# Optimization experiments

Measured on AMD Instinct MI355X. Metric: run time of the kernel, lower is better.

Reference implementation:

```python
import jax, jax.numpy as jnp
import numpy as np

N, E = 50000, 800000          # nodes, edges
DIN, HEAD, HD = 128, 4, 16    # input dim, heads, per-head dim
DOUT = HEAD * HD              # 64 = head*hd
NEG_SLOPE = 0.01              # torch LeakyReLU default


def _lin(key, fan_in, fan_out):
    # torch nn.Linear default init: U(-1/sqrt(fan_in), 1/sqrt(fan_in))
    kw, kb = jax.random.split(key)
    s = 1.0 / np.sqrt(fan_in)
    W = jax.random.uniform(kw, (fan_in, fan_out), jnp.float32, -s, s)
    b = jax.random.uniform(kb, (fan_out,), jnp.float32, -s, s)
    return W, b


def setup_inputs() -> dict:
    key = jax.random.key(0)
    ks = jax.random.split(key, 8)
    x = jax.random.normal(ks[0], (N, DIN), jnp.float32)
    src = jax.random.randint(ks[1], (E,), 0, N, jnp.int32)
    dst = jax.random.randint(ks[2], (E,), 0, N, jnp.int32)
    Ws, bs = _lin(ks[3], DIN, DOUT)   # relation_aware src linear
    Wd, bd = _lin(ks[4], DIN, DOUT)   # relation_aware dst linear
    Wl, bl = _lin(ks[5], DIN, DOUT)   # w_liner
    Wa, ba = _lin(ks[6], 3 * HD, 1)   # atten
    return dict(x=x, src=src, dst=dst, Ws=Ws, bs=bs, Wd=Wd, bd=bd,
                Wl=Wl, bl=bl, Wa=Wa, ba=ba)


def reference(x, src, dst, Ws, bs, Wd, bd, Wl, bl, Wa, ba):
    # sign_edges: relation-aware per-edge feature edge_sum  [E, DOUT]
    er = jnp.tanh(x[src] @ Ws + bs + (x[dst] @ Wd + bd))

    # w_liner on node features  [N, DOUT]
    h = x @ Wl + bl

    # message: per-edge, per-head concat + linear + leakyrelu score
    sf = h[src].reshape(E, HEAD, HD)
    df = h[dst].reshape(E, HEAD, HD)
    ef = er.reshape(E, HEAD, HD)
    z = jnp.concatenate([sf, df, ef], axis=-1)        # [E, HEAD, 3*HD]
    a = z @ Wa + ba                                    # [E, HEAD, 1]
    a = jnp.where(a >= 0, a, NEG_SLOPE * a)            # leaky relu

    # reduce: mailbox softmax over incoming edges of each dst node
    m = jax.ops.segment_max(a, dst, num_segments=N)    # [N, HEAD, 1]
    m = jnp.where(jnp.isfinite(m), m, 0.0)             # empty mailboxes -> 0
    e = jnp.exp(a - m[dst])
    s = jax.ops.segment_sum(e, dst, num_segments=N)    # [N, HEAD, 1]
    attn = e / jnp.maximum(s[dst], 1e-38)

    out = jax.ops.segment_sum(attn * sf, dst, num_segments=N)
    out = out.reshape(N, DOUT)                         # [N, head*hd]

    # edge_s: mean of edge_sum over incoming edges per node
    deg = jax.ops.segment_sum(jnp.ones((E, 1), x.dtype), dst, num_segments=N)
    edge_s = jax.ops.segment_sum(er, dst, num_segments=N) / jnp.maximum(deg, 1.0)

    return (edge_s, out, h)  # if_sum=False branch: h already [N, head*hd]
```

## Files before the change

### kernel.cpp

```cpp
#include <hip/hip_runtime.h>
#include <math.h>

#define DIN   128
#define DOUT  64
#define NHEAD 4
#define HD    16

typedef __attribute__((ext_vector_type(8))) short bf16x8;
typedef __attribute__((ext_vector_type(8))) unsigned short u16x8;
typedef __attribute__((ext_vector_type(4))) float f32x4;

__device__ __forceinline__ unsigned short f2bf(float f) {
    union { float f; unsigned u; } v; v.f = f;
    unsigned r = v.u + 0x7FFF + ((v.u >> 16) & 1);
    return (unsigned short)(r >> 16);
}
__device__ __forceinline__ float bf2f(unsigned short s) {
    union { unsigned u; float f; } v; v.u = ((unsigned)s) << 16; return v.f;
}

__global__ __launch_bounds__(256)
void k_prep(const float* __restrict__ Ws, const float* __restrict__ Wd,
            const float* __restrict__ Wl, short* __restrict__ wT,
            int* __restrict__ degi, int N) {
    const int idx = blockIdx.x * 256 + threadIdx.x;
    if (idx < 192 * 128) {
        const int n = idx >> 7, k = idx & 127;
        float v;
        if (n < 64)       v = Ws[k * DOUT + n];
        else if (n < 128) v = Wd[k * DOUT + (n - 64)];
        else              v = Wl[k * DOUT + (n - 128)];
        wT[idx] = (short)f2bf(v);
    }
    if (idx < N) degi[idx] = 0;
}

__global__ __launch_bounds__(64)
void k_node_proj(const float* __restrict__ x, const short* __restrict__ wT,
                 const float* __restrict__ bs, const float* __restrict__ bd,
                 const float* __restrict__ bl, const float* __restrict__ Wa,
                 unsigned short* __restrict__ packed_bf,
                 float* __restrict__ xd,
                 float* __restrict__ alpha_s, float* __restrict__ alpha_d,
                 float* __restrict__ h_out, int N) {
    __shared__ short xs[16 * 136];
    const int lane = threadIdx.x;
    const int lam = lane & 15, g = lane >> 4;
    const int n0 = blockIdx.x * 16;

    {
        const int r = lane >> 2, c0 = (lane & 3) * 32;
        const int nn = n0 + r;
#pragma unroll
        for (int j = 0; j < 8; ++j) {
            float4 v = make_float4(0.f, 0.f, 0.f, 0.f);
            if (nn < N) v = ((const float4*)x)[(size_t)nn * 32 + (c0 >> 2) + j];
            short4 h4;
            h4.x = (short)f2bf(v.x); h4.y = (short)f2bf(v.y);
            h4.z = (short)f2bf(v.z); h4.w = (short)f2bf(v.w);
            *(short4*)&xs[r * 136 + c0 + j * 4] = h4;
        }
    }
    __syncthreads();

    bf16x8 afr[4];
#pragma unroll
    for (int ks = 0; ks < 4; ++ks)
        afr[ks] = *(const bf16x8*)&xs[lam * 136 + ks * 32 + g * 8];

    f32x4 acc[12];
#pragma unroll
    for (int c = 0; c < 12; ++c) acc[c] = (f32x4){0.f, 0.f, 0.f, 0.f};

#pragma unroll
    for (int c = 0; c < 12; ++c) {
#pragma unroll
        for (int ks = 0; ks < 4; ++ks) {
            const bf16x8 b = *(const bf16x8*)&wT[(c * 16 + lam) * 128 + ks * 32 + g * 8];
            acc[c] = __builtin_amdgcn_mfma_f32_16x16x32_bf16(afr[ks], b, acc[c], 0, 0, 0);
        }
    }

    float bsv[4], bdv[4], blv[4];
#pragma unroll
    for (int c = 0; c < 4; ++c) {
        bsv[c] = bs[c * 16 + lam];
        bdv[c] = bd[c * 16 + lam];
        blv[c] = bl[c * 16 + lam];
    }
    const float waS = Wa[lam], waD = Wa[16 + lam];
    const int cc_base = (lam >> 2), t_sl = lam & 3;

#pragma unroll
    for (int i = 0; i < 4; ++i) {
        const int node = n0 + g * 4 + i;
        float xsv[4], xdv[4], hv[4];
#pragma unroll
        for (int c = 0; c < 4; ++c) {
            xsv[c] = acc[c][i]     + bsv[c];
            xdv[c] = acc[4 + c][i] + bdv[c];
            hv[c]  = acc[8 + c][i] + blv[c];
        }
        float p0 = hv[0] * waS, p1 = hv[1] * waS, p2 = hv[2] * waS, p3 = hv[3] * waS;
        float q0 = hv[0] * waD, q1 = hv[1] * waD, q2 = hv[2] * waD, q3 = hv[3] * waD;
#pragma unroll
        for (int off = 1; off < 16; off <<= 1) {
            p0 += __shfl_xor(p0, off); p1 += __shfl_xor(p1, off);
            p2 += __shfl_xor(p2, off); p3 += __shfl_xor(p3, off);
            q0 += __shfl_xor(q0, off); q1 += __shfl_xor(q1, off);
            q2 += __shfl_xor(q2, off); q3 += __shfl_xor(q3, off);
        }
        if (node < N) {
            const size_t rowb = (size_t)node * 128;
#pragma unroll
            for (int c = 0; c < 4; ++c) {
                const int cc = c * 4 + cc_base;
                packed_bf[rowb + cc * 8 + t_sl]     = f2bf(xsv[c]);
                packed_bf[rowb + cc * 8 + 4 + t_sl] = f2bf(hv[c]);
                xd   [(size_t)node * DOUT + c * 16 + lam] = xdv[c];
                h_out[(size_t)node * DOUT + c * 16 + lam] = hv[c];
            }
            if (lam == 0) {
                *(f32x4*)&alpha_s[(size_t)node * NHEAD] = (f32x4){p0, p1, p2, p3};
                *(f32x4*)&alpha_d[(size_t)node * NHEAD] = (f32x4){q0, q1, q2, q3};
            }
        }
    }
}

__global__ __launch_bounds__(256)
void k_hist(const int* __restrict__ dst, int* __restrict__ degi,
            int* __restrict__ rank, int E) {
    const int e0 = (blockIdx.x * 256 + threadIdx.x) * 4;
    if (e0 + 3 < E) {
        const int4 d = *(const int4*)&dst[e0];
        int4 r;
        r.x = atomicAdd(&degi[d.x], 1);
        r.y = atomicAdd(&degi[d.y], 1);
        r.z = atomicAdd(&degi[d.z], 1);
        r.w = atomicAdd(&degi[d.w], 1);
        *(int4*)&rank[e0] = r;
    } else {
        for (int e = e0; e < E; ++e) rank[e] = atomicAdd(&degi[dst[e]], 1);
    }
}

__global__ __launch_bounds__(1024)
void k_scan_block(const int* __restrict__ degi, int* __restrict__ excl,
                  int* __restrict__ bsum, int N) {
    __shared__ int wsum[16];
    const int tid = threadIdx.x, lane = tid & 63, wid = tid >> 6;
    const int i = blockIdx.x * 1024 + tid;
    int v = (i < N) ? degi[i] : 0;
    int incl = v;
#pragma unroll
    for (int off = 1; off < 64; off <<= 1) {
        int t = __shfl_up(incl, off);
        if (lane >= off) incl += t;
    }
    if (lane == 63) wsum[wid] = incl;
    __syncthreads();
    if (tid < 16) {
        int t = wsum[tid];
#pragma unroll
        for (int off = 1; off < 16; off <<= 1) {
            int u = __shfl_up(t, off);
            if (tid >= off) t += u;
        }
        wsum[tid] = t;
    }
    __syncthreads();
    const int base = (wid > 0) ? wsum[wid - 1] : 0;
    if (i < N) excl[i] = incl - v + base;
    if (tid == 1023) bsum[blockIdx.x] = wsum[15];
}

__global__ __launch_bounds__(1024)
void k_scan_bsum(const int* __restrict__ bsum, int* __restrict__ boff,
                 int* __restrict__ total, int nb) {
    __shared__ int wsum[16];
    const int tid = threadIdx.x, lane = tid & 63, wid = tid >> 6;
    int v = (tid < nb) ? bsum[tid] : 0;
    int incl = v;
#pragma unroll
    for (int off = 1; off < 64; off <<= 1) {
        int t = __shfl_up(incl, off);
        if (lane >= off) incl += t;
    }
    if (lane == 63) wsum[wid] = incl;
    __syncthreads();
    if (tid < 16) {
        int t = wsum[tid];
#pragma unroll
        for (int off = 1; off < 16; off <<= 1) {
            int u = __shfl_up(t, off);
            if (tid >= off) t += u;
        }
        wsum[tid] = t;
    }
    __syncthreads();
    const int base = (wid > 0) ? wsum[wid - 1] : 0;
    if (tid < nb) boff[tid] = incl - v + base;
    if (tid == 1023) *total = wsum[15];
}

__global__ __launch_bounds__(256)
void k_scatter(const int* __restrict__ src, const int* __restrict__ dst,
               const int* __restrict__ rp_raw, const int* __restrict__ boff,
               const int* __restrict__ rank, int* __restrict__ srcs_sorted, int E) {
    const int e0 = (blockIdx.x * 256 + threadIdx.x) * 4;
    if (e0 + 3 < E) {
        const int4 s = *(const int4*)&src[e0];
        const int4 d = *(const int4*)&dst[e0];
        const int4 r = *(const int4*)&rank[e0];
        srcs_sorted[rp_raw[d.x] + boff[d.x >> 10] + r.x] = s.x;
        srcs_sorted[rp_raw[d.y] + boff[d.y >> 10] + r.y] = s.y;
        srcs_sorted[rp_raw[d.z] + boff[d.z >> 10] + r.z] = s.z;
        srcs_sorted[rp_raw[d.w] + boff[d.w >> 10] + r.w] = s.w;
    } else {
        for (int e = e0; e < E; ++e) {
            const int d = dst[e];
            srcs_sorted[rp_raw[d] + boff[d >> 10] + rank[e]] = src[e];
        }
    }
}

__global__ __launch_bounds__(256, 8)
void k_aggregate(const int* __restrict__ rp_raw, const int* __restrict__ boff,
                 const int* __restrict__ total, const int* __restrict__ srcs,
                 const unsigned short* __restrict__ packed_bf,
                 const float* __restrict__ xd,
                 const float* __restrict__ alpha_s, const float* __restrict__ alpha_d,
                 const float* __restrict__ Wa, const float* __restrict__ ba,
                 float* __restrict__ edge_s, float* __restrict__ out, int N) {
    const int lane = threadIdx.x & 63;
    const int n = blockIdx.x * 4 + (threadIdx.x >> 6);
    if (n >= N) return;
    const int g = lane >> 4, lam = lane & 15;
    const int hd = lam >> 2, q = lam & 3;

    const int start = rp_raw[n] + boff[n >> 10];
    const int end = (n + 1 < N) ? (rp_raw[n + 1] + boff[(n + 1) >> 10]) : *total;
    const int deg = end - start;
    const int last = end - 1;

    const float4 xd4 = *(const float4*)&xd[(size_t)n * DOUT + lam * 4];
    const float4 wa4 = *(const float4*)&Wa[32 + q * 4];
    const float adb  = alpha_d[n * NHEAD + hd] + ba[0];

    float es0=0.f,es1=0.f,es2=0.f,es3=0.f;
    float o0=0.f,o1=0.f,o2=0.f,o3=0.f;
    float s = 0.f;

    const int niter = (deg + 3) >> 2;
    int e = start + g;

    float vm0 = 0.f, vm1 = 0.f;
    u16x8 pk0 = (u16x8){0,0,0,0,0,0,0,0}, pk1 = pk0;
    float as0 = 0.f, as1 = 0.f;
    if (niter > 0) {
        vm0 = (e < end) ? 1.f : 0.f;
        const int sn = srcs[min(e, last)];
        pk0 = *(const u16x8*)&packed_bf[(size_t)sn * 128 + lam * 8];
        as0 = alpha_s[sn * NHEAD + hd];
        const int e1 = e + 4;
        vm1 = (e1 < end) ? 1.f : 0.f;
        const int sn1 = srcs[min(e1, last)];
        pk1 = *(const u16x8*)&packed_bf[(size_t)sn1 * 128 + lam * 8];
        as1 = alpha_s[sn1 * NHEAD + hd];
    }

    for (int it = 0; it < niter; ++it) {
        float vmn = 0.f, asn = 0.f;
        u16x8 pkn = (u16x8){0,0,0,0,0,0,0,0};
        const int e2 = e + 8;
        if (it + 2 < niter) {
            vmn = (e2 < end) ? 1.f : 0.f;
            const int sn = srcs[min(e2, last)];
            pkn = *(const u16x8*)&packed_bf[(size_t)sn * 128 + lam * 8];
            asn = alpha_s[sn * NHEAD + hd];
        }

        const float t0 = __expf(2.f * (bf2f(pk0[0]) + xd4.x));
        const float t1 = __expf(2.f * (bf2f(pk0[1]) + xd4.y));
        const float t2 = __expf(2.f * (bf2f(pk0[2]) + xd4.z));
        const float t3 = __expf(2.f * (bf2f(pk0[3]) + xd4.w));
        const float er0 = fmaf(-2.f, __builtin_amdgcn_rcpf(t0 + 1.f), 1.f);
        const float er1 = fmaf(-2.f, __builtin_amdgcn_rcpf(t1 + 1.f), 1.f);
        const float er2 = fmaf(-2.f, __builtin_amdgcn_rcpf(t2 + 1.f), 1.f);
        const float er3 = fmaf(-2.f, __builtin_amdgcn_rcpf(t3 + 1.f), 1.f);
        es0 = fmaf(er0, vm0, es0); es1 = fmaf(er1, vm0, es1);
        es2 = fmaf(er2, vm0, es2); es3 = fmaf(er3, vm0, es3);

        float p = er0 * wa4.x;
        p = fmaf(er1, wa4.y, p);
        p = fmaf(er2, wa4.z, p);
        p = fmaf(er3, wa4.w, p);
        p += __shfl_xor(p, 1);
        p += __shfl_xor(p, 2);

        float a = as0 + adb + p;
        a = (a >= 0.f) ? a : 0.01f * a;
        const float w = __expf(a) * vm0;
        s += w;
        o0 = fmaf(w, bf2f(pk0[4]), o0); o1 = fmaf(w, bf2f(pk0[5]), o1);
        o2 = fmaf(w, bf2f(pk0[6]), o2); o3 = fmaf(w, bf2f(pk0[7]), o3);

        vm0 = vm1; pk0 = pk1; as0 = as1;
        vm1 = vmn; pk1 = pkn; as1 = asn;
        e += 4;
    }

#pragma unroll
    for (int off = 16; off < 64; off <<= 1) {
        es0 += __shfl_xor(es0, off); es1 += __shfl_xor(es1, off);
        es2 += __shfl_xor(es2, off); es3 += __shfl_xor(es3, off);
        o0  += __shfl_xor(o0,  off); o1  += __shfl_xor(o1,  off);
        o2  += __shfl_xor(o2,  off); o3  += __shfl_xor(o3,  off);
        s   += __shfl_xor(s,   off);
    }

    if (g == 0) {
        const float inv_s = __builtin_amdgcn_rcpf(fmaxf(s, 1e-38f));
        const float inv_d = __builtin_amdgcn_rcpf(fmaxf((float)deg, 1.0f));
        const size_t od = (size_t)n * DOUT + lam * 4;
        *(f32x4*)&out[od]    = (f32x4){o0 * inv_s, o1 * inv_s, o2 * inv_s, o3 * inv_s};
        *(f32x4*)&edge_s[od] = (f32x4){es0 * inv_d, es1 * inv_d, es2 * inv_d, es3 * inv_d};
    }
}

extern "C" void kernel_launch(void* const* d_in, const int* in_sizes, int n_in,
                              void* d_out, int out_size, void* d_ws, size_t ws_size,
                              hipStream_t stream) {
    const float* x  = (const float*)d_in[0];
    const int*   src= (const int*)  d_in[1];
    const int*   dst= (const int*)  d_in[2];
    const float* Ws = (const float*)d_in[3];
    const float* bs = (const float*)d_in[4];
    const float* Wd = (const float*)d_in[5];
    const float* bd = (const float*)d_in[6];
    const float* Wl = (const float*)d_in[7];
    const float* bl = (const float*)d_in[8];
    const float* Wa = (const float*)d_in[9];
    const float* ba = (const float*)d_in[10];

    const int N = in_sizes[0] / DIN;
    const int E = in_sizes[1];
    const int NB = (N + 1023) / 1024;

    float* out_f = (float*)d_out;
    float* edge_s_out = out_f;
    float* out_attn   = out_f + (size_t)N * DOUT;
    float* h_out      = out_f + 2 * (size_t)N * DOUT;

    char* ws = (char*)d_ws;
    size_t o = 0;
    unsigned short* packed_bf = (unsigned short*)(ws + o); o += (size_t)N * 128 * 2;
    float* xd      = (float*)(ws + o); o += (size_t)N * DOUT * 4;
    float* alpha_s = (float*)(ws + o); o += (size_t)N * NHEAD * 4;
    float* alpha_d = (float*)(ws + o); o += (size_t)N * NHEAD * 4;
    int*   degi    = (int*)  (ws + o); o += (size_t)N * 4;
    int*   rp_raw  = (int*)  (ws + o); o += (size_t)(N + 1) * 4;
    int*   rank    = (int*)  (ws + o); o += (size_t)E * 4;
    int*   srcs    = (int*)  (ws + o); o += (size_t)E * 4;
    int*   bsum    = (int*)  (ws + o); o += (size_t)NB * 4;
    int*   boff    = (int*)  (ws + o); o += (size_t)NB * 4;
    int*   total   = (int*)  (ws + o); o += 64;
    short* wT      = (short*)(ws + o); o += (size_t)192 * 128 * 2;

    const int prep_n = (N > 192 * 128) ? N : 192 * 128;
    k_prep<<<(prep_n + 255) / 256, 256, 0, stream>>>(Ws, Wd, Wl, wT, degi, N);

    k_node_proj<<<(N + 15) / 16, 64, 0, stream>>>(x, wT, bs, bd, bl, Wa,
                                                  packed_bf, xd, alpha_s, alpha_d,
                                                  h_out, N);

    k_hist<<<((E + 3) / 4 + 255) / 256, 256, 0, stream>>>(dst, degi, rank, E);

    k_scan_block<<<NB, 1024, 0, stream>>>(degi, rp_raw, bsum, N);
    k_scan_bsum<<<1, 1024, 0, stream>>>(bsum, boff, total, NB);

    k_scatter<<<((E + 3) / 4 + 255) / 256, 256, 0, stream>>>(src, dst, rp_raw, boff,
                                                             rank, srcs, E);

    k_aggregate<<<(N + 3) / 4, 256, 0, stream>>>(rp_raw, boff, total, srcs,
                                                 packed_bf, xd,
                                                 alpha_s, alpha_d, Wa, ba,
                                                 edge_s_out, out_attn, N);
}
```

Before: 137.8 us.

## Fuse prep/hist, single-pass scan, interleave projection with scatter, deepen prefetch

Merges weight transpose with the degree histogram, and replaces the two-kernel scan with one kernel that uses a last-block atomic counter for the block-offset scan. The node projection now runs in 256-thread blocks of 64 nodes and stages packed bf16 rows in shared memory so global writes are coalesced, and it is interleaved with the edge scatter in one launch. The aggregate loop prefetch depth grows from two to three. The aim is fewer launches, fewer serial kernel boundaries and better latency hiding, at the cost of more registers and a scan that assumes at most 64 blocks.

```diff
diff --git a/kernel.cpp b/kernel.cpp
--- a/kernel.cpp
+++ b/kernel.cpp
@@ -20,118 +20,22 @@
 }
 
 __global__ __launch_bounds__(256)
-void k_prep(const float* __restrict__ Ws, const float* __restrict__ Wd,
-            const float* __restrict__ Wl, short* __restrict__ wT,
-            int* __restrict__ degi, int N) {
-    const int idx = blockIdx.x * 256 + threadIdx.x;
-    if (idx < 192 * 128) {
+void k_prep_hist(const float* __restrict__ Ws, const float* __restrict__ Wd,
+                 const float* __restrict__ Wl, short* __restrict__ wT,
+                 const int* __restrict__ dst, int* __restrict__ degi,
+                 int* __restrict__ rank, int E) {
+    const int bid = blockIdx.x, tid = threadIdx.x;
+    if (bid < 96) {
+        const int idx = bid * 256 + tid;
         const int n = idx >> 7, k = idx & 127;
         float v;
         if (n < 64)       v = Ws[k * DOUT + n];
         else if (n < 128) v = Wd[k * DOUT + (n - 64)];
         else              v = Wl[k * DOUT + (n - 128)];
         wT[idx] = (short)f2bf(v);
-    }
-    if (idx < N) degi[idx] = 0;
-}
-
-__global__ __launch_bounds__(64)
-void k_node_proj(const float* __restrict__ x, const short* __restrict__ wT,
-                 const float* __restrict__ bs, const float* __restrict__ bd,
-                 const float* __restrict__ bl, const float* __restrict__ Wa,
-                 unsigned short* __restrict__ packed_bf,
-                 float* __restrict__ xd,
-                 float* __restrict__ alpha_s, float* __restrict__ alpha_d,
-                 float* __restrict__ h_out, int N) {
-    __shared__ short xs[16 * 136];
-    const int lane = threadIdx.x;
-    const int lam = lane & 15, g = lane >> 4;
-    const int n0 = blockIdx.x * 16;
-
-    {
-        const int r = lane >> 2, c0 = (lane & 3) * 32;
-        const int nn = n0 + r;
-#pragma unroll
-        for (int j = 0; j < 8; ++j) {
-            float4 v = make_float4(0.f, 0.f, 0.f, 0.f);
-            if (nn < N) v = ((const float4*)x)[(size_t)nn * 32 + (c0 >> 2) + j];
-            short4 h4;
-            h4.x = (short)f2bf(v.x); h4.y = (short)f2bf(v.y);
-            h4.z = (short)f2bf(v.z); h4.w = (short)f2bf(v.w);
-            *(short4*)&xs[r * 136 + c0 + j * 4] = h4;
-        }
-    }
-    __syncthreads();
-
-    bf16x8 afr[4];
-#pragma unroll
-    for (int ks = 0; ks < 4; ++ks)
-        afr[ks] = *(const bf16x8*)&xs[lam * 136 + ks * 32 + g * 8];
-
-    f32x4 acc[12];
-#pragma unroll
-    for (int c = 0; c < 12; ++c) acc[c] = (f32x4){0.f, 0.f, 0.f, 0.f};
-
-#pragma unroll
-    for (int c = 0; c < 12; ++c) {
-#pragma unroll
-        for (int ks = 0; ks < 4; ++ks) {
-            const bf16x8 b = *(const bf16x8*)&wT[(c * 16 + lam) * 128 + ks * 32 + g * 8];
-            acc[c] = __builtin_amdgcn_mfma_f32_16x16x32_bf16(afr[ks], b, acc[c], 0, 0, 0);
-        }
-    }
-
-    float bsv[4], bdv[4], blv[4];
-#pragma unroll
-    for (int c = 0; c < 4; ++c) {
-        bsv[c] = bs[c * 16 + lam];
-        bdv[c] = bd[c * 16 + lam];
-        blv[c] = bl[c * 16 + lam];
-    }
-    const float waS = Wa[lam], waD = Wa[16 + lam];
-    const int cc_base = (lam >> 2), t_sl = lam & 3;
-
-#pragma unroll
-    for (int i = 0; i < 4; ++i) {
-        const int node = n0 + g * 4 + i;
-        float xsv[4], xdv[4], hv[4];
-#pragma unroll
-        for (int c = 0; c < 4; ++c) {
-            xsv[c] = acc[c][i]     + bsv[c];
-            xdv[c] = acc[4 + c][i] + bdv[c];
-            hv[c]  = acc[8 + c][i] + blv[c];
-        }
-        float p0 = hv[0] * waS, p1 = hv[1] * waS, p2 = hv[2] * waS, p3 = hv[3] * waS;
-        float q0 = hv[0] * waD, q1 = hv[1] * waD, q2 = hv[2] * waD, q3 = hv[3] * waD;
-#pragma unroll
-        for (int off = 1; off < 16; off <<= 1) {
-            p0 += __shfl_xor(p0, off); p1 += __shfl_xor(p1, off);
-            p2 += __shfl_xor(p2, off); p3 += __shfl_xor(p3, off);
-            q0 += __shfl_xor(q0, off); q1 += __shfl_xor(q1, off);
-            q2 += __shfl_xor(q2, off); q3 += __shfl_xor(q3, off);
-        }
-        if (node < N) {
-            const size_t rowb = (size_t)node * 128;
-#pragma unroll
-            for (int c = 0; c < 4; ++c) {
-                const int cc = c * 4 + cc_base;
-                packed_bf[rowb + cc * 8 + t_sl]     = f2bf(xsv[c]);
-                packed_bf[rowb + cc * 8 + 4 + t_sl] = f2bf(hv[c]);
-                xd   [(size_t)node * DOUT + c * 16 + lam] = xdv[c];
-                h_out[(size_t)node * DOUT + c * 16 + lam] = hv[c];
-            }
-            if (lam == 0) {
-                *(f32x4*)&alpha_s[(size_t)node * NHEAD] = (f32x4){p0, p1, p2, p3};
-                *(f32x4*)&alpha_d[(size_t)node * NHEAD] = (f32x4){q0, q1, q2, q3};
-            }
-        }
-    }
-}
-
-__global__ __launch_bounds__(256)
-void k_hist(const int* __restrict__ dst, int* __restrict__ degi,
-            int* __restrict__ rank, int E) {
-    const int e0 = (blockIdx.x * 256 + threadIdx.x) * 4;
+        return;
+    }
+    const int e0 = ((bid - 96) * 256 + tid) * 4;
     if (e0 + 3 < E) {
         const int4 d = *(const int4*)&dst[e0];
         int4 r;
@@ -146,9 +50,11 @@
 }
 
 __global__ __launch_bounds__(1024)
-void k_scan_block(const int* __restrict__ degi, int* __restrict__ excl,
-                  int* __restrict__ bsum, int N) {
+void k_scan(const int* __restrict__ degi, int* __restrict__ excl,
+            int* __restrict__ bsum, int* __restrict__ boff,
+            int* __restrict__ total, int* __restrict__ counter, int N, int NB) {
     __shared__ int wsum[16];
+    __shared__ int amLast;
     const int tid = threadIdx.x, lane = tid & 63, wid = tid >> 6;
     const int i = blockIdx.x * 1024 + tid;
     int v = (i < N) ? degi[i] : 0;
@@ -172,55 +78,157 @@
     __syncthreads();
     const int base = (wid > 0) ? wsum[wid - 1] : 0;
     if (i < N) excl[i] = incl - v + base;
-    if (tid == 1023) bsum[blockIdx.x] = wsum[15];
-}
-
-__global__ __launch_bounds__(1024)
-void k_scan_bsum(const int* __restrict__ bsum, int* __restrict__ boff,
-                 int* __restrict__ total, int nb) {
-    __shared__ int wsum[16];
-    const int tid = threadIdx.x, lane = tid & 63, wid = tid >> 6;
-    int v = (tid < nb) ? bsum[tid] : 0;
-    int incl = v;
-#pragma unroll
-    for (int off = 1; off < 64; off <<= 1) {
-        int t = __shfl_up(incl, off);
-        if (lane >= off) incl += t;
-    }
-    if (lane == 63) wsum[wid] = incl;
-    __syncthreads();
-    if (tid < 16) {
-        int t = wsum[tid];
+    if (tid == 1023) atomicExch(&bsum[blockIdx.x], wsum[15]);
+    __syncthreads();
+    if (tid == 0) {
+        __threadfence();
+        amLast = (atomicAdd(counter, 1) == NB - 1) ? 1 : 0;
+    }
+    __syncthreads();
+    if (amLast && tid < 64) {
+        int b = (tid < NB) ? atomicAdd(&bsum[tid], 0) : 0;
+        int inc = b;
+#pragma unroll
+        for (int off = 1; off < 64; off <<= 1) {
+            int t = __shfl_up(inc, off);
+            if (lane >= off) inc += t;
+        }
+        if (tid < NB) boff[tid] = inc - b;
+        if (tid == 63) *total = inc;
+    }
+}
+
+__global__ __launch_bounds__(256)
+void k_proj_scatter(const float* __restrict__ x, const short* __restrict__ wT,
+                    const float* __restrict__ bs, const float* __restrict__ bd,
+                    const float* __restrict__ bl, const float* __restrict__ Wa,
+                    unsigned short* __restrict__ packed_bf,
+                    float* __restrict__ xd, float* __restrict__ alpha_s,
+                    float* __restrict__ alpha_d, float* __restrict__ h_out, int N,
+                    const int* __restrict__ src, const int* __restrict__ dst,
+                    const int* __restrict__ rp_raw, const int* __restrict__ boff,
+                    const int* __restrict__ rank, int* __restrict__ srcs_sorted,
+                    int E, int NPJ, int NSC) {
+    __shared__ short xs[64 * 136];
+    const int bid = blockIdx.x, tid = threadIdx.x;
+
+    if (bid & 1) {
+        const int sb = bid >> 1;
+        if (sb >= NSC) return;
+        const int e0 = (sb * 256 + tid) * 4;
+        if (e0 + 3 < E) {
+            const int4 s = *(const int4*)&src[e0];
+            const int4 d = *(const int4*)&dst[e0];
+            const int4 r = *(const int4*)&rank[e0];
+            srcs_sorted[rp_raw[d.x] + boff[d.x >> 10] + r.x] = s.x;
+            srcs_sorted[rp_raw[d.y] + boff[d.y >> 10] + r.y] = s.y;
+            srcs_sorted[rp_raw[d.z] + boff[d.z >> 10] + r.z] = s.z;
+            srcs_sorted[rp_raw[d.w] + boff[d.w >> 10] + r.w] = s.w;
+        } else {
+            for (int e = e0; e < E && e >= 0; ++e) {
+                const int d = dst[e];
+                srcs_sorted[rp_raw[d] + boff[d >> 10] + rank[e]] = src[e];
+            }
+        }
+        return;
+    }
+
+    const int pb = bid >> 1;
+    if (pb >= NPJ) return;
+    const int wave = tid >> 6, lane = tid & 63;
+    const int lam = lane & 15, g = lane >> 4;
+    const int n0 = pb * 64;
+
+    {
+        const int r = tid >> 2, c0 = (tid & 3) * 32;
+        const int nn = n0 + r;
+#pragma unroll
+        for (int j = 0; j < 8; ++j) {
+            float4 v = make_float4(0.f, 0.f, 0.f, 0.f);
+            if (nn < N) v = ((const float4*)x)[(size_t)nn * 32 + (c0 >> 2) + j];
+            short4 h4;
+            h4.x = (short)f2bf(v.x); h4.y = (short)f2bf(v.y);
+            h4.z = (short)f2bf(v.z); h4.w = (short)f2bf(v.w);
+            *(short4*)&xs[r * 136 + c0 + j * 4] = h4;
+        }
+    }
+    __syncthreads();
+
+    bf16x8 afr[4];
+#pragma unroll
+    for (int ks = 0; ks < 4; ++ks)
+        afr[ks] = *(const bf16x8*)&xs[(wave * 16 + lam) * 136 + ks * 32 + g * 8];
+    __syncthreads();
+
+    f32x4 acc[12];
+#pragma unroll
+    for (int c = 0; c < 12; ++c) acc[c] = (f32x4){0.f, 0.f, 0.f, 0.f};
+#pragma unroll
+    for (int c = 0; c < 12; ++c) {
+#pragma unroll
+        for (int ks = 0; ks < 4; ++ks) {
+            const bf16x8 b = *(const bf16x8*)&wT[(c * 16 + lam) * 128 + ks * 32 + g * 8];
+            acc[c] = __builtin_amdgcn_mfma_f32_16x16x32_bf16(afr[ks], b, acc[c], 0, 0, 0);
+        }
+    }
+
+    float bsv[4], bdv[4], blv[4];
+#pragma unroll
+    for (int c = 0; c < 4; ++c) {
+        bsv[c] = bs[c * 16 + lam];
+        bdv[c] = bd[c * 16 + lam];
+        blv[c] = bl[c * 16 + lam];
+    }
+    const float waS = Wa[lam], waD = Wa[16 + lam];
+    const int cc_base = lam >> 2, t_sl = lam & 3;
+
+#pragma unroll
+    for (int i = 0; i < 4; ++i) {
+        const int node = n0 + wave * 16 + g * 4 + i;
+        const int lrow = (wave * 16 + g * 4 + i) * 128;
+        float xsv[4], xdv[4], hv[4];
+#pragma unroll
+        for (int c = 0; c < 4; ++c) {
+            xsv[c] = acc[c][i]     + bsv[c];
+            xdv[c] = acc[4 + c][i] + bdv[c];
+            hv[c]  = acc[8 + c][i] + blv[c];
+        }
+        float p0 = hv[0] * waS, p1 = hv[1] * waS, p2 = hv[2] * waS, p3 = hv[3] * waS;
+        float q0 = hv[0] * waD, q1 = hv[1] * waD, q2 = hv[2] * waD, q3 = hv[3] * waD;
 #pragma unroll
         for (int off = 1; off < 16; off <<= 1) {
-            int u = __shfl_up(t, off);
-            if (tid >= off) t += u;
-        }
-        wsum[tid] = t;
-    }
-    __syncthreads();
-    const int base = (wid > 0) ? wsum[wid - 1] : 0;
-    if (tid < nb) boff[tid] = incl - v + base;
-    if (tid == 1023) *total = wsum[15];
-}
-
-__global__ __launch_bounds__(256)
-void k_scatter(const int* __restrict__ src, const int* __restrict__ dst,
-               const int* __restrict__ rp_raw, const int* __restrict__ boff,
-               const int* __restrict__ rank, int* __restrict__ srcs_sorted, int E) {
-    const int e0 = (blockIdx.x * 256 + threadIdx.x) * 4;
-    if (e0 + 3 < E) {
-        const int4 s = *(const int4*)&src[e0];
-        const int4 d = *(const int4*)&dst[e0];
-        const int4 r = *(const int4*)&rank[e0];
-        srcs_sorted[rp_raw[d.x] + boff[d.x >> 10] + r.x] = s.x;
-        srcs_sorted[rp_raw[d.y] + boff[d.y >> 10] + r.y] = s.y;
-        srcs_sorted[rp_raw[d.z] + boff[d.z >> 10] + r.z] = s.z;
-        srcs_sorted[rp_raw[d.w] + boff[d.w >> 10] + r.w] = s.w;
-    } else {
-        for (int e = e0; e < E; ++e) {
-            const int d = dst[e];
-            srcs_sorted[rp_raw[d] + boff[d >> 10] + rank[e]] = src[e];
+            p0 += __shfl_xor(p0, off); p1 += __shfl_xor(p1, off);
+            p2 += __shfl_xor(p2, off); p3 += __shfl_xor(p3, off);
+            q0 += __shfl_xor(q0, off); q1 += __shfl_xor(q1, off);
+            q2 += __shfl_xor(q2, off); q3 += __shfl_xor(q3, off);
+        }
+#pragma unroll
+        for (int c = 0; c < 4; ++c) {
+            const int cc = c * 4 + cc_base;
+            xs[lrow + cc * 8 + t_sl]     = (short)f2bf(xsv[c]);
+            xs[lrow + cc * 8 + 4 + t_sl] = (short)f2bf(hv[c]);
+        }
+        if (node < N) {
+#pragma unroll
+            for (int c = 0; c < 4; ++c) {
+                xd   [(size_t)node * DOUT + c * 16 + lam] = xdv[c];
+                h_out[(size_t)node * DOUT + c * 16 + lam] = hv[c];
+            }
+            if (lam == 0) {
+                *(f32x4*)&alpha_s[(size_t)node * NHEAD] = (f32x4){p0, p1, p2, p3};
+                *(f32x4*)&alpha_d[(size_t)node * NHEAD] = (f32x4){q0, q1, q2, q3};
+            }
+        }
+    }
+    __syncthreads();
+#pragma unroll
+    for (int k = 0; k < 4; ++k) {
+        const int ci = k * 256 + tid;
+        const int ln = ci >> 4, sub = ci & 15;
+        const int node = n0 + ln;
+        if (node < N) {
+            const u16x8 vv = *(const u16x8*)&xs[ln * 128 + sub * 8];
+            *(u16x8*)&packed_bf[(size_t)node * 128 + sub * 8] = vv;
         }
     }
 }
@@ -255,28 +263,39 @@
     const int niter = (deg + 3) >> 2;
     int e = start + g;
 
-    float vm0 = 0.f, vm1 = 0.f;
-    u16x8 pk0 = (u16x8){0,0,0,0,0,0,0,0}, pk1 = pk0;
-    float as0 = 0.f, as1 = 0.f;
+    float vm0=0.f, vm1=0.f, vm2=0.f;
+    u16x8 pk0=(u16x8){0,0,0,0,0,0,0,0}, pk1=pk0, pk2=pk0;
+    float as0=0.f, as1=0.f, as2=0.f;
     if (niter > 0) {
-        vm0 = (e < end) ? 1.f : 0.f;
-        const int sn = srcs[min(e, last)];
-        pk0 = *(const u16x8*)&packed_bf[(size_t)sn * 128 + lam * 8];
-        as0 = alpha_s[sn * NHEAD + hd];
-        const int e1 = e + 4;
-        vm1 = (e1 < end) ? 1.f : 0.f;
-        const int sn1 = srcs[min(e1, last)];
-        pk1 = *(const u16x8*)&packed_bf[(size_t)sn1 * 128 + lam * 8];
-        as1 = alpha_s[sn1 * NHEAD + hd];
+        {
+            vm0 = (e < end) ? 1.f : 0.f;
+            const int sn = srcs[min(e, last)];
+            pk0 = *(const u16x8*)&packed_bf[(size_t)sn * 128 + lam * 8];
+            as0 = alpha_s[sn * NHEAD + hd];
+        }
+        {
+            const int e1 = e + 4;
+            vm1 = (e1 < end) ? 1.f : 0.f;
+            const int sn = srcs[min(e1, last)];
+            pk1 = *(const u16x8*)&packed_bf[(size_t)sn * 128 + lam * 8];
+            as1 = alpha_s[sn * NHEAD + hd];
+        }
+        {
+            const int e2 = e + 8;
+            vm2 = (e2 < end) ? 1.f : 0.f;
+            const int sn = srcs[min(e2, last)];
+            pk2 = *(const u16x8*)&packed_bf[(size_t)sn * 128 + lam * 8];
+            as2 = alpha_s[sn * NHEAD + hd];
+        }
     }
 
     for (int it = 0; it < niter; ++it) {
         float vmn = 0.f, asn = 0.f;
         u16x8 pkn = (u16x8){0,0,0,0,0,0,0,0};
-        const int e2 = e + 8;
-        if (it + 2 < niter) {
-            vmn = (e2 < end) ? 1.f : 0.f;
-            const int sn = srcs[min(e2, last)];
+        const int e3 = e + 12;
+        if (it + 3 < niter) {
+            vmn = (e3 < end) ? 1.f : 0.f;
+            const int sn = srcs[min(e3, last)];
             pkn = *(const u16x8*)&packed_bf[(size_t)sn * 128 + lam * 8];
             asn = alpha_s[sn * NHEAD + hd];
         }
@@ -307,7 +326,8 @@
         o2 = fmaf(w, bf2f(pk0[6]), o2); o3 = fmaf(w, bf2f(pk0[7]), o3);
 
         vm0 = vm1; pk0 = pk1; as0 = as1;
-        vm1 = vmn; pk1 = pkn; as1 = asn;
+        vm1 = vm2; pk1 = pk2; as1 = as2;
+        vm2 = vmn; pk2 = pkn; as2 = asn;
         e += 4;
     }
 
@@ -360,28 +380,29 @@
     float* alpha_s = (float*)(ws + o); o += (size_t)N * NHEAD * 4;
     float* alpha_d = (float*)(ws + o); o += (size_t)N * NHEAD * 4;
     int*   degi    = (int*)  (ws + o); o += (size_t)N * 4;
+    int*   counter = (int*)  (ws + o); o += 64;
     int*   rp_raw  = (int*)  (ws + o); o += (size_t)(N + 1) * 4;
     int*   rank    = (int*)  (ws + o); o += (size_t)E * 4;
     int*   srcs    = (int*)  (ws + o); o += (size_t)E * 4;
-    int*   bsum    = (int*)  (ws + o); o += (size_t)NB * 4;
-    int*   boff    = (int*)  (ws + o); o += (size_t)NB * 4;
+    int*   bsum    = (int*)  (ws + o); o += 64 * 4;
+    int*   boff    = (int*)  (ws + o); o += 64 * 4;
     int*   total   = (int*)  (ws + o); o += 64;
     short* wT      = (short*)(ws + o); o += (size_t)192 * 128 * 2;
 
-    const int prep_n = (N > 192 * 128) ? N : 192 * 128;
-    k_prep<<<(prep_n + 255) / 256, 256, 0, stream>>>(Ws, Wd, Wl, wT, degi, N);
-
-    k_node_proj<<<(N + 15) / 16, 64, 0, stream>>>(x, wT, bs, bd, bl, Wa,
-                                                  packed_bf, xd, alpha_s, alpha_d,
-                                                  h_out, N);
-
-    k_hist<<<((E + 3) / 4 + 255) / 256, 256, 0, stream>>>(dst, degi, rank, E);
-
-    k_scan_block<<<NB, 1024, 0, stream>>>(degi, rp_raw, bsum, N);
-    k_scan_bsum<<<1, 1024, 0, stream>>>(bsum, boff, total, NB);
-
-    k_scatter<<<((E + 3) / 4 + 255) / 256, 256, 0, stream>>>(src, dst, rp_raw, boff,
-                                                             rank, srcs, E);
+    hipMemsetAsync(degi, 0, (size_t)N * 4 + 64, stream);
+
+    const int HB = (E + 1023) / 1024;
+    k_prep_hist<<<96 + HB, 256, 0, stream>>>(Ws, Wd, Wl, wT, dst, degi, rank, E);
+
+    k_scan<<<NB, 1024, 0, stream>>>(degi, rp_raw, bsum, boff, total, counter, N, NB);
+
+    const int NPJ = (N + 63) / 64;
+    const int NSC = (E + 1023) / 1024;
+    const int GC  = 2 * ((NPJ > NSC) ? NPJ : NSC);
+    k_proj_scatter<<<GC, 256, 0, stream>>>(x, wT, bs, bd, bl, Wa,
+                                           packed_bf, xd, alpha_s, alpha_d, h_out, N,
+                                           src, dst, rp_raw, boff, rank, srcs,
+                                           E, NPJ, NSC);
 
     k_aggregate<<<(N + 3) / 4, 256, 0, stream>>>(rp_raw, boff, total, srcs,
                                                  packed_bf, xd,
```

After: 154.5 us. +12.1%, slower.
